# Kernel optimization log

Measured on AMD Instinct MI355X. Metric: run time of the kernel, lower is better.

Reference implementation:

```python
import jax, jax.numpy as jnp
import numpy as np


def setup_inputs() -> dict:
    key = jax.random.key(0)
    ks = jax.random.split(key, 3)
    B, d_in, d_latent = 8192, 768, 12288
    x = jax.random.normal(ks[0], (B, d_in), dtype=jnp.float32)
    # kaiming_normal fan_in relu: std = sqrt(2/d_in)
    W_enc = jax.random.normal(ks[1], (d_latent, d_in), dtype=jnp.float32) * np.sqrt(2.0 / d_in)
    b_enc = jnp.zeros((d_latent,), dtype=jnp.float32)
    # xavier_normal: std = sqrt(2/(d_in+d_latent))
    W_dec = jax.random.normal(ks[2], (d_in, d_latent), dtype=jnp.float32) * np.sqrt(2.0 / (d_in + d_latent))
    b_dec = jnp.zeros((d_in,), dtype=jnp.float32)
    b_pre = jnp.zeros((d_in,), dtype=jnp.float32)
    return {"x": x, "b_pre": b_pre, "W_enc": W_enc, "b_enc": b_enc,
            "W_dec": W_dec, "b_dec": b_dec, "k": 64}


def reference(x, b_pre, W_enc, b_enc, W_dec, b_dec, k):
    # encode: a = (x - b_pre) @ W_enc.T + b_enc   -> (B, d_latent)
    x0 = x - b_pre
    a = jnp.einsum('bi,li->bl', x0, W_enc) + b_enc
    # topk activation (mode='value', nonneg=True): relu then keep k largest
    a_relu = jax.nn.relu(a)
    topk_val, topk_idx = jax.lax.top_k(a_relu, k)  # (B, k)
    B = a.shape[0]
    rows = jnp.arange(B)[:, None]
    z = jnp.zeros_like(a).at[rows, topk_idx].set(topk_val)
    # decode: x_hat = z @ W_dec.T + b_dec
    x_hat = jnp.einsum('bl,il->bi', z, W_dec) + b_dec
    return (x_hat, z, a)
```

## Files before the change

kernel.cpp:

```cpp
#include <hip/hip_runtime.h>

#define DIN 768
#define DL  12288
#define CAP 320
#define CAP2 512
#define WCAP 256
#define TCAND 2.9f
#define MARGIN 0.03f
#define UB 0.015f
#define UMAX 64
#define KMAX 128

typedef __attribute__((ext_vector_type(8))) _Float16 half8;
typedef __attribute__((ext_vector_type(4))) _Float16 half4v;
typedef __attribute__((ext_vector_type(4))) float f32x4;

__device__ __forceinline__ void gl_lds16(const void* g, void* s) {
  __builtin_amdgcn_global_load_lds(
      (const __attribute__((address_space(1))) unsigned int*)g,
      (__attribute__((address_space(3))) unsigned int*)s, 16, 0, 0);
}
__device__ __forceinline__ void wait_lgkm0_fence() {
  asm volatile("s_waitcnt lgkmcnt(0)" ::: "memory");
  __builtin_amdgcn_sched_barrier(0);
}
__device__ __forceinline__ void wait_vm0() {
  asm volatile("s_waitcnt vmcnt(0)" ::: "memory");
}

#define NBX (8192 * DIN / 1024)
#define NBW (DL * DIN / 1024)
#define NBT ((DL / 32) * (DIN / 32))

template <int ZMETA>
__global__ __launch_bounds__(256) void k_prep(
    const float* __restrict__ x, const float* __restrict__ b_pre,
    const float* __restrict__ W_enc, const float* __restrict__ W_dec,
    _Float16* __restrict__ Ah, _Float16* __restrict__ Bh, _Float16* __restrict__ WT,
    int* __restrict__ meta)
{
  const int b = blockIdx.x, tid = threadIdx.x;
  if (b < NBX) {
    const int i4 = b * 256 + tid;
    const int col4 = (i4 % (DIN / 4)) * 4;
    const float4 xv = *(const float4*)&x[(size_t)i4 * 4];
    const float4 bp = *(const float4*)&b_pre[col4];
    half4v o;
    o.x = (_Float16)(xv.x - bp.x);
    o.y = (_Float16)(xv.y - bp.y);
    o.z = (_Float16)(xv.z - bp.z);
    o.w = (_Float16)(xv.w - bp.w);
    *(half4v*)&Ah[(size_t)i4 * 4] = o;
  } else if (b < NBX + NBW) {
    const int i4 = (b - NBX) * 256 + tid;
    const float4 wv = *(const float4*)&W_enc[(size_t)i4 * 4];
    half4v o;
    o.x = (_Float16)wv.x; o.y = (_Float16)wv.y;
    o.z = (_Float16)wv.z; o.w = (_Float16)wv.w;
    *(half4v*)&Bh[(size_t)i4 * 4] = o;
  } else if (b < NBX + NBW + NBT) {
    const int idx = b - NBX - NBW;
    const int c0 = (idx % (DL / 32)) * 32;
    const int r0 = (idx / (DL / 32)) * 32;
    const int xx = tid & 31, yy = tid >> 5;
    __shared__ float t[32][33];
#pragma unroll
    for (int dy = 0; dy < 32; dy += 8)
      t[yy + dy][xx] = W_dec[(size_t)(r0 + yy + dy) * DL + c0 + xx];
    __syncthreads();
#pragma unroll
    for (int dy = 0; dy < 32; dy += 8)
      WT[(size_t)(c0 + yy + dy) * DIN + r0 + xx] = (_Float16)t[xx][yy + dy];
  } else if (ZMETA) {
    const int4 z4 = {0, 0, 0, 0};
#pragma unroll
    for (int s = 0; s < 16; ++s) ((int4*)meta)[tid * 16 + s] = z4;
  }
}

#define BM 256
#define BN 256
#define BKE 64
#define NKT (DIN / BKE)

template <int EMIT>
__global__ __launch_bounds__(512) void k_encode_f16(
    const _Float16* __restrict__ Ah, const _Float16* __restrict__ Bh,
    const float* __restrict__ b_enc, float* __restrict__ aout,
    int* __restrict__ cnt, int2* __restrict__ cand)
{
  __shared__ _Float16 sA[2][BM][BKE];
  __shared__ _Float16 sB[2][BN][BKE];
  __shared__ int s_bcnt8[8];
  __shared__ int s_ovf;
  const int tid = threadIdx.x, wave = tid >> 6, lane = tid & 63;
  const int wm = wave >> 2, wn = wave & 3;
  const int fr = lane & 15, fc = lane >> 4;

  const int q = ((8192 / BM) * (DL / BN)) >> 3;
  const int wg = (blockIdx.x & 7) * q + (blockIdx.x >> 3);
  const int bm = (wg / (DL / BN)) * BM;
  const int bn = (wg % (DL / BN)) * BN;

  const int lrow = lane >> 3;
  const int lcol = ((lane & 7) ^ lrow) << 3;
  const _Float16* gA = Ah + (size_t)(bm + lrow) * DIN + lcol;
  const _Float16* gB = Bh + (size_t)(bn + lrow) * DIN + lcol;

  f32x4 acc[8][4];
#pragma unroll
  for (int i = 0; i < 8; ++i)
#pragma unroll
    for (int j = 0; j < 4; ++j) acc[i][j] = f32x4{0.f, 0.f, 0.f, 0.f};

#define STAGE_TILE(buf, tt)                                                      \
  {                                                                              \
    _Pragma("unroll")                                                            \
    for (int s4 = 0; s4 < 4; ++s4) {                                             \
      const int s8 = (wave + s4 * 8) * 8;                                        \
      gl_lds16(gA + (size_t)s8 * DIN + (tt) * BKE, &sA[buf][s8][0]);             \
      gl_lds16(gB + (size_t)s8 * DIN + (tt) * BKE, &sB[buf][s8][0]);             \
    }                                                                            \
  }

#define LOAD_AF(p, mh)                                                           \
  {                                                                              \
    const char* bA = (const char*)&sA[p][0][0];                                  \
    _Pragma("unroll")                                                            \
    for (int i = 0; i < 4; ++i)                                                  \
      _Pragma("unroll")                                                          \
      for (int ks = 0; ks < 2; ++ks) {                                           \
        const int row = wm * 128 + ((mh) * 4 + i) * 16 + fr;                     \
        const int ph = (ks * 4 + fc) ^ (fr & 7);                                 \
        af[i][ks] = *(const half8*)(bA + row * (BKE * 2) + ph * 16);             \
      }                                                                          \
  }
#define LOAD_BF(p, nh)                                                           \
  {                                                                              \
    const char* bB = (const char*)&sB[p][0][0];                                  \
    _Pragma("unroll")                                                            \
    for (int j = 0; j < 2; ++j)                                                  \
      _Pragma("unroll")                                                          \
      for (int ks = 0; ks < 2; ++ks) {                                           \
        const int row = wn * 64 + ((nh) * 2 + j) * 16 + fr;                      \
        const int ph = (ks * 4 + fc) ^ (fr & 7);                                 \
        bf[nh][j][ks] = *(const half8*)(bB + row * (BKE * 2) + ph * 16);         \
      }                                                                          \
  }

#define MFMAQ(mh, nh)                                                            \
  __builtin_amdgcn_s_setprio(1);                                                 \
  _Pragma("unroll")                                                              \
  for (int i = 0; i < 4; ++i)                                                    \
    _Pragma("unroll")                                                            \
    for (int j = 0; j < 2; ++j)                                                  \
      _Pragma("unroll")                                                          \
      for (int ks = 0; ks < 2; ++ks)                                             \
        acc[(mh) * 4 + i][(nh) * 2 + j] = __builtin_amdgcn_mfma_f32_16x16x32_f16( \
            af[i][ks], bf[nh][j][ks], acc[(mh) * 4 + i][(nh) * 2 + j], 0, 0, 0); \
  __builtin_amdgcn_s_setprio(0);

  half8 af[4][2], bf[2][2][2];

  STAGE_TILE(0, 0)
  wait_vm0();
  __builtin_amdgcn_s_barrier();

#pragma unroll 1
  for (int t = 0; t < NKT; ++t) {
    const int p = t & 1;
    LOAD_AF(p, 0)
    LOAD_BF(p, 0)
    if (t + 1 < NKT) STAGE_TILE(p ^ 1, t + 1)
    __builtin_amdgcn_s_barrier();
    wait_lgkm0_fence();
    MFMAQ(0, 0)
    __builtin_amdgcn_s_barrier();
    LOAD_BF(p, 1)
    __builtin_amdgcn_s_barrier();
    wait_lgkm0_fence();
    MFMAQ(0, 1)
    __builtin_amdgcn_s_barrier();
    LOAD_AF(p, 1)
    wait_vm0();
    __builtin_amdgcn_s_barrier();
    wait_lgkm0_fence();
    MFMAQ(1, 1)
    MFMAQ(1, 0)
    __builtin_amdgcn_s_barrier();
  }

  unsigned* pk   = (unsigned*)&sA[0][0][0];
  float*    pv   = (float*)&sA[1][0][0];
  int*      lcnt = (int*)&sB[0][0][0];
  if (EMIT) {
    if (tid < 8) s_bcnt8[tid] = 0;
    if (tid == 0) s_ovf = 0;
    if (tid < 256) lcnt[tid] = 0;
    __syncthreads();
  }

#pragma unroll
  for (int j = 0; j < 4; ++j) {
    const int col = bn + wn * 64 + j * 16 + fr;
    const float be = b_enc[col];
#pragma unroll
    for (int i = 0; i < 8; ++i) {
      const int row0 = bm + wm * 128 + i * 16 + fc * 4;
#pragma unroll
      for (int r = 0; r < 4; ++r) {
        const float v = acc[i][j][r] + be;
        aout[(size_t)(row0 + r) * DL + col] = v;
        if (EMIT && v > TCAND) {
          const int lr = wm * 128 + i * 16 + fc * 4 + r;
          const int lc = wn * 64 + j * 16 + fr;
          const int p2 = atomicAdd(&s_bcnt8[wave], 1);
          if (p2 < WCAP) {
            pk[wave * WCAP + p2] = ((unsigned)lr << 8) | (unsigned)lc;
            pv[wave * WCAP + p2] = v;
          }
          atomicAdd(&lcnt[lr], 1);
        }
      }
    }
  }

  if (EMIT) {
    __syncthreads();
    if (tid < 8 && s_bcnt8[tid] > WCAP) s_ovf = 1;
    __syncthreads();
    if (s_ovf) {
      if (tid < 256) atomicAdd(&cnt[bm + tid], CAP2);
    } else {
      if (tid < 256) {
        const int c = lcnt[tid];
        lcnt[tid] = c ? atomicAdd(&cnt[bm + tid], c) : 0;
      }
      __syncthreads();
#pragma unroll 1
      for (int w = 0; w < 8; ++w) {
        const int tw = s_bcnt8[w];
        for (int e = tid; e < tw; e += 512) {
          const unsigned pkv = pk[w * WCAP + e];
          const int lr = pkv >> 8, lc = pkv & 255u;
          const int p2 = atomicAdd(&lcnt[lr], 1);
          if (p2 < CAP2) {
            int2 o; o.x = __float_as_int(pv[w * WCAP + e]); o.y = bn + lc;
            cand[(size_t)(bm + lr) * CAP2 + p2] = o;
          }
        }
      }
    }
  }
#undef STAGE_TILE
#undef LOAD_AF
#undef LOAD_BF
#undef MFMAQ
}

__global__ __launch_bounds__(512) void k_fast(
    const int* __restrict__ cnt, const int2* __restrict__ cand,
    const float* __restrict__ x, const float* __restrict__ b_pre,
    const float* __restrict__ W, const float* __restrict__ b_enc,
    const int* __restrict__ kp, const _Float16* __restrict__ WT,
    const float* __restrict__ b_dec, float* __restrict__ z,
    float* __restrict__ xhat, int* __restrict__ flag)
{
  const int row = blockIdx.x, tid = threadIdx.x;
  const int wave = tid >> 6, lane = tid & 63;
  const int kk = min(max(kp[0], 1), KMAX);
  float* zr = z + (size_t)row * DL;

  __shared__ float cv[CAP2];
  __shared__ int ci[CAP2];
  __shared__ double x0[DIN];
  __shared__ float s_ak;
  __shared__ int s_nw, s_ucnt;
  __shared__ int uidx[UMAX];
  __shared__ double uex[UMAX];
  __shared__ int widx[KMAX];
  __shared__ float wval[KMAX];

  const float4 zz = {0.f, 0.f, 0.f, 0.f};
#pragma unroll
  for (int j = 0; j < 6; ++j) ((float4*)zr)[tid + 512 * j] = zz;

  const int Craw = cnt[row];
  const int C = min(Craw, CAP2);
  for (int i = tid; i < C; i += 512) {
    const int2 p = cand[(size_t)row * CAP2 + i];
    cv[i] = __int_as_float(p.x);
    ci[i] = p.y;
  }
  for (int i = tid; i < DIN; i += 512)
    x0[i] = (double)x[(size_t)row * DIN + i] - (double)b_pre[i];
  if (tid == 0) { s_ak = -1e30f; s_nw = 0; s_ucnt = 0; }
  __syncthreads();

  bool defic = (Craw >= CAP2) || (C < kk);
  if (!defic) {
    if (tid < C) {
      const float mv = cv[tid];
      const int mi = ci[tid];
      int r = 0;
      for (int j = 0; j < C; ++j) {
        const float fj = cv[j];
        if (fj > mv || (fj == mv && ci[j] < mi)) ++r;
      }
      if (r == kk - 1) s_ak = mv;
    }
    __syncthreads();
    if (s_ak - UB <= TCAND) defic = true;
  } else {
    __syncthreads();
  }
  if (defic) {
    if (tid == 0) flag[row] = 1;
    return;
  }
  const float ak = s_ak;

  if (tid < C) {
    const float mv = cv[tid];
    if (mv > ak + UB) {
      const int p = atomicAdd(&s_nw, 1);
      widx[p] = ci[tid]; wval[p] = mv;
    } else if (mv >= ak - UB) {
      const int p = atomicAdd(&s_ucnt, 1);
      if (p < UMAX) uidx[p] = ci[tid];
    }
  }
  __syncthreads();
  const int nci = s_nw;
  const int ucnt = min(s_ucnt, UMAX);

  for (int c = wave; c < ucnt; c += 8) {
    const int idx = uidx[c];
    const float* wrow = W + (size_t)idx * DIN;
    double s = 0.0;
#pragma unroll
    for (int it = 0; it < DIN / 64; ++it)
      s = fma(x0[lane + it * 64], (double)wrow[lane + it * 64], s);
#pragma unroll
    for (int mm = 32; mm; mm >>= 1) s += __shfl_xor(s, mm);
    if (lane == 0) {
      const double e = s + (double)b_enc[idx];
      uex[c] = e > 0.0 ? e : 0.0;
    }
  }
  __syncthreads();

  const int utake = min(kk - nci, ucnt);
  if (tid < ucnt) {
    const double mv = uex[tid];
    const int mi = uidx[tid];
    int r = 0;
    for (int j = 0; j < ucnt; ++j) {
      const double fj = uex[j];
      if (fj > mv || (fj == mv && uidx[j] < mi)) ++r;
    }
    if (r < utake) {
      const int p = atomicAdd(&s_nw, 1);
      widx[p] = mi; wval[p] = (float)mv;
    }
  }
  __syncthreads();
  const int nW = s_nw;

  if (tid < nW) zr[widx[tid]] = wval[tid];

  if (tid < 192) {
    float4 acc = ((const float4*)b_dec)[tid];
    for (int j = 0; j < nW; ++j) {
      const float vv = wval[j];
      const half4v w4 = *(const half4v*)(WT + (size_t)widx[j] * DIN + tid * 4);
      acc.x = fmaf(vv, (float)w4.x, acc.x);
      acc.y = fmaf(vv, (float)w4.y, acc.y);
      acc.z = fmaf(vv, (float)w4.z, acc.z);
      acc.w = fmaf(vv, (float)w4.w, acc.w);
    }
    ((float4*)(xhat + (size_t)row * DIN))[tid] = acc;
  }
}

template <int FORCE_ALL, int ZERO_Z>
__global__ __launch_bounds__(512) void k_full(
    const float* __restrict__ a, const float* __restrict__ x,
    const float* __restrict__ b_pre, const float* __restrict__ W,
    const float* __restrict__ b_enc, const int* __restrict__ kp,
    const _Float16* __restrict__ WT, const float* __restrict__ b_dec,
    float* __restrict__ z, float* __restrict__ xhat, const int* __restrict__ flag)
{
  const int row = blockIdx.x, tid = threadIdx.x;
  if (!FORCE_ALL && flag[row] == 0) return;
  const int wave = tid >> 6, lane = tid & 63;
  const int kk = min(max(kp[0], 1), KMAX);
  const float* ar = a + (size_t)row * DL;
  float* zr = z + (size_t)row * DL;

  __shared__ unsigned hist[4][512];
  __shared__ float s_wmax[8];
  __shared__ unsigned s_wsuf[8];
  __shared__ float s_Tm;
  __shared__ int s_cnt;
  __shared__ int cidx[CAP];
  __shared__ float caf[CAP];
  __shared__ double x0[DIN];
  __shared__ float s_ak;
  __shared__ int s_ucnt, s_nw;
  __shared__ int uidx[UMAX];
  __shared__ double uex[UMAX];
  __shared__ int widx[KMAX];
  __shared__ float wval[KMAX];

  float4 v[6];
#pragma unroll
  for (int j = 0; j < 6; ++j) {
    float4 t4 = ((const float4*)ar)[tid + 512 * j];
    t4.x = fmaxf(t4.x, 0.f); t4.y = fmaxf(t4.y, 0.f);
    t4.z = fmaxf(t4.z, 0.f); t4.w = fmaxf(t4.w, 0.f);
    v[j] = t4;
    if (ZERO_Z) {
      const float4 zz = {0.f, 0.f, 0.f, 0.f};
      ((float4*)zr)[tid + 512 * j] = zz;
    }
  }
  for (int i = tid; i < DIN; i += 512)
    x0[i] = (double)x[(size_t)row * DIN + i] - (double)b_pre[i];
  float m = 0.f;
#pragma unroll
  for (int j = 0; j < 6; ++j)
    m = fmaxf(m, fmaxf(fmaxf(v[j].x, v[j].y), fmaxf(v[j].z, v[j].w)));
#pragma unroll
  for (int off = 32; off; off >>= 1) m = fmaxf(m, __shfl_xor(m, off));
  if (lane == 0) s_wmax[wave] = m;
  if (tid == 0) { s_cnt = 0; s_Tm = -1.f; s_ak = -1e30f; s_ucnt = 0; s_nw = 0; }
  __syncthreads();
  float rmax = s_wmax[0];
#pragma unroll
  for (int w2 = 1; w2 < 8; ++w2) rmax = fmaxf(rmax, s_wmax[w2]);

  float Tm;
  if (rmax <= 0.f) {
    Tm = 1e30f;
  } else {
    const float scale = 512.f / rmax;
    unsigned need = (unsigned)kk;
    bool found = false;
    for (int phase = 0; phase < 2 && !found; ++phase) {
      for (int i = tid; i < 4 * 512; i += 512) (&hist[0][0])[i] = 0u;
      __syncthreads();
      unsigned* h = hist[wave & 3];
      const float sc = (phase == 0) ? scale : scale * 8.f;
#pragma unroll
      for (int j = 0; j < 6; ++j) {
        const float vv[4] = {v[j].x, v[j].y, v[j].z, v[j].w};
#pragma unroll
        for (int e = 0; e < 4; ++e) {
          const float val = vv[e];
          if (val > 0.f) {
            const float fb = val * scale;
            if (phase == 0) {
              if (fb >= 64.f) atomicAdd(&h[min(511, (int)fb)], 1u);
            } else {
              if (fb < 64.f) atomicAdd(&h[min(511, (int)(val * sc))], 1u);
            }
          }
        }
      }
      __syncthreads();
      const unsigned st = hist[0][tid] + hist[1][tid] + hist[2][tid] + hist[3][tid];
      unsigned s = st;
#pragma unroll
      for (int off = 1; off < 64; off <<= 1) {
        const unsigned o = __shfl_down(s, off);
        if (lane + off < 64) s += o;
      }
      if (lane == 0) s_wsuf[wave] = s;
      __syncthreads();
      unsigned above_w = 0, total = 0;
#pragma unroll
      for (int w2 = 0; w2 < 8; ++w2) {
        total += s_wsuf[w2];
        if (w2 > wave) above_w += s_wsuf[w2];
      }
      const unsigned inc = s + above_w;
      const unsigned excl = inc - st;
      if (total >= need) {
        if (inc >= need && excl < need)
          s_Tm = (float)tid / sc - MARGIN;
        found = true;
      } else {
        need -= total;
      }
      __syncthreads();
    }
    Tm = s_Tm;
  }

#pragma unroll
  for (int j = 0; j < 6; ++j) {
    const float vv[4] = {v[j].x, v[j].y, v[j].z, v[j].w};
#pragma unroll
    for (int e = 0; e < 4; ++e) {
      if (vv[e] > 0.f && vv[e] >= Tm) {
        const int p = atomicAdd(&s_cnt, 1);
        if (p < CAP) { cidx[p] = (tid + 512 * j) * 4 + e; caf[p] = vv[e]; }
      }
    }
  }
  __syncthreads();
  const int C = min(s_cnt, CAP);

  if (C > kk) {
    if (tid < C) {
      const float mv = caf[tid];
      const int mi = cidx[tid];
      int r = 0;
      for (int j = 0; j < C; ++j) {
        const float fj = caf[j];
        if (fj > mv || (fj == mv && cidx[j] < mi)) ++r;
      }
      if (r == kk - 1) s_ak = mv;
    }
    __syncthreads();
  }
  const float ak = s_ak;

  if (tid < C) {
    const float mv = caf[tid];
    if (C <= kk || mv > ak + UB) {
      const int p = atomicAdd(&s_nw, 1);
      widx[p] = cidx[tid]; wval[p] = mv;
    } else if (mv >= ak - UB) {
      const int p = atomicAdd(&s_ucnt, 1);
      if (p < UMAX) uidx[p] = cidx[tid];
    }
  }
  __syncthreads();
  const int nci = s_nw;
  const int ucnt = min(s_ucnt, UMAX);

  for (int c = wave; c < ucnt; c += 8) {
    const int idx = uidx[c];
    const float* wrow = W + (size_t)idx * DIN;
    double s = 0.0;
#pragma unroll
    for (int it = 0; it < DIN / 64; ++it)
      s = fma(x0[lane + it * 64], (double)wrow[lane + it * 64], s);
#pragma unroll
    for (int mm = 32; mm; mm >>= 1) s += __shfl_xor(s, mm);
    if (lane == 0) {
      const double e = s + (double)b_enc[idx];
      uex[c] = e > 0.0 ? e : 0.0;
    }
  }
  __syncthreads();

  const int utake = min(kk - nci, ucnt);
  if (tid < ucnt) {
    const double mv = uex[tid];
    const int mi = uidx[tid];
    int r = 0;
    for (int j = 0; j < ucnt; ++j) {
      const double fj = uex[j];
      if (fj > mv || (fj == mv && uidx[j] < mi)) ++r;
    }
    if (r < utake) {
      const int p = atomicAdd(&s_nw, 1);
      widx[p] = mi; wval[p] = (float)mv;
    }
  }
  __syncthreads();
  const int nW = s_nw;

  if (tid < nW) zr[widx[tid]] = wval[tid];

  if (tid < 192) {
    float4 acc = ((const float4*)b_dec)[tid];
    for (int j = 0; j < nW; ++j) {
      const float vv = wval[j];
      const half4v w4 = *(const half4v*)(WT + (size_t)widx[j] * DIN + tid * 4);
      acc.x = fmaf(vv, (float)w4.x, acc.x);
      acc.y = fmaf(vv, (float)w4.y, acc.y);
      acc.z = fmaf(vv, (float)w4.z, acc.z);
      acc.w = fmaf(vv, (float)w4.w, acc.w);
    }
    ((float4*)(xhat + (size_t)row * DIN))[tid] = acc;
  }
}

extern "C" void kernel_launch(void* const* d_in, const int* in_sizes, int n_in,
                              void* d_out, int out_size, void* d_ws, size_t ws_size,
                              hipStream_t stream)
{
  const float* x     = (const float*)d_in[0];
  const float* b_pre = (const float*)d_in[1];
  const float* W_enc = (const float*)d_in[2];
  const float* b_enc = (const float*)d_in[3];
  const float* W_dec = (const float*)d_in[4];
  const float* b_dec = (const float*)d_in[5];
  const int*   kp    = (const int*)d_in[6];
  const int M = in_sizes[0] / DIN;

  float* xhat = (float*)d_out;
  float* z    = xhat + (size_t)M * DIN;
  float* a    = z + (size_t)M * DL;

  const bool bigws = ws_size >= ((size_t)192 << 20);

  if (bigws) {
    int*      cnt  = (int*)d_ws;
    int*      flag = (int*)d_ws + M;
    int2*     cand = (int2*)((char*)d_ws + ((size_t)1 << 20));
    _Float16* WT16 = (_Float16*)((char*)d_ws + ((size_t)40 << 20));
    _Float16* Ah   = (_Float16*)((char*)d_ws + ((size_t)64 << 20));
    _Float16* Bh   = (_Float16*)((char*)d_ws + ((size_t)96 << 20));

    k_prep<1><<<NBX + NBW + NBT + 1, 256, 0, stream>>>(x, b_pre, W_enc, W_dec,
                                                       Ah, Bh, WT16, cnt);
    k_encode_f16<1><<<(M / BM) * (DL / BN), 512, 0, stream>>>(Ah, Bh, b_enc, a,
                                                              cnt, cand);
    k_fast<<<M, 512, 0, stream>>>(cnt, cand, x, b_pre, W_enc, b_enc, kp, WT16, b_dec,
                                  z, xhat, flag);
    k_full<0, 0><<<M, 512, 0, stream>>>(a, x, b_pre, W_enc, b_enc, kp, WT16, b_dec,
                                        z, xhat, flag);
  } else {
    _Float16* WT16 = (_Float16*)z;
    _Float16* Ah   = (_Float16*)(z + (size_t)12 * 1024 * 1024);
    _Float16* Bh   = (_Float16*)(z + (size_t)20 * 1024 * 1024);

    k_prep<0><<<NBX + NBW + NBT, 256, 0, stream>>>(x, b_pre, W_enc, W_dec,
                                                   Ah, Bh, WT16, nullptr);
    k_encode_f16<0><<<(M / BM) * (DL / BN), 512, 0, stream>>>(Ah, Bh, b_enc, a,
                                                              nullptr, nullptr);
    k_full<1, 1><<<M, 512, 0, stream>>>(a, x, b_pre, W_enc, b_enc, kp, WT16, b_dec,
                                        z, xhat, nullptr);
  }
}
```

Measured before the change: 630.7 us.

## Merge fast and fallback top-k kernels; simplify encode GEMM barriers

```diff
diff --git a/kernel.cpp b/kernel.cpp
--- a/kernel.cpp
+++ b/kernel.cpp
@@ -19,13 +19,6 @@
   __builtin_amdgcn_global_load_lds(
       (const __attribute__((address_space(1))) unsigned int*)g,
       (__attribute__((address_space(3))) unsigned int*)s, 16, 0, 0);
-}
-__device__ __forceinline__ void wait_lgkm0_fence() {
-  asm volatile("s_waitcnt lgkmcnt(0)" ::: "memory");
-  __builtin_amdgcn_sched_barrier(0);
-}
-__device__ __forceinline__ void wait_vm0() {
-  asm volatile("s_waitcnt vmcnt(0)" ::: "memory");
 }
 
 #define NBX (8192 * DIN / 1024)
@@ -74,7 +67,7 @@
   } else if (ZMETA) {
     const int4 z4 = {0, 0, 0, 0};
 #pragma unroll
-    for (int s = 0; s < 16; ++s) ((int4*)meta)[tid * 16 + s] = z4;
+    for (int s = 0; s < 8; ++s) ((int4*)meta)[tid * 8 + s] = z4;
   }
 }
 
@@ -163,8 +156,7 @@
   half8 af[4][2], bf[2][2][2];
 
   STAGE_TILE(0, 0)
-  wait_vm0();
-  __builtin_amdgcn_s_barrier();
+  __syncthreads();
 
 #pragma unroll 1
   for (int t = 0; t < NKT; ++t) {
@@ -172,22 +164,13 @@
     LOAD_AF(p, 0)
     LOAD_BF(p, 0)
     if (t + 1 < NKT) STAGE_TILE(p ^ 1, t + 1)
-    __builtin_amdgcn_s_barrier();
-    wait_lgkm0_fence();
     MFMAQ(0, 0)
-    __builtin_amdgcn_s_barrier();
     LOAD_BF(p, 1)
-    __builtin_amdgcn_s_barrier();
-    wait_lgkm0_fence();
     MFMAQ(0, 1)
-    __builtin_amdgcn_s_barrier();
     LOAD_AF(p, 1)
-    wait_vm0();
-    __builtin_amdgcn_s_barrier();
-    wait_lgkm0_fence();
     MFMAQ(1, 1)
     MFMAQ(1, 0)
-    __builtin_amdgcn_s_barrier();
+    __syncthreads();
   }
 
   unsigned* pk   = (unsigned*)&sA[0][0][0];
@@ -258,13 +241,13 @@
 #undef MFMAQ
 }
 
-__global__ __launch_bounds__(512) void k_fast(
+__global__ __launch_bounds__(512) void k_back(
     const int* __restrict__ cnt, const int2* __restrict__ cand,
-    const float* __restrict__ x, const float* __restrict__ b_pre,
-    const float* __restrict__ W, const float* __restrict__ b_enc,
-    const int* __restrict__ kp, const _Float16* __restrict__ WT,
-    const float* __restrict__ b_dec, float* __restrict__ z,
-    float* __restrict__ xhat, int* __restrict__ flag)
+    const float* __restrict__ a, const float* __restrict__ x,
+    const float* __restrict__ b_pre, const float* __restrict__ W,
+    const float* __restrict__ b_enc, const int* __restrict__ kp,
+    const _Float16* __restrict__ WT, const float* __restrict__ b_dec,
+    float* __restrict__ z, float* __restrict__ xhat)
 {
   const int row = blockIdx.x, tid = threadIdx.x;
   const int wave = tid >> 6, lane = tid & 63;
@@ -275,18 +258,22 @@
   __shared__ int ci[CAP2];
   __shared__ double x0[DIN];
   __shared__ float s_ak;
-  __shared__ int s_nw, s_ucnt;
+  __shared__ int s_nw, s_ucnt, s_cnt2;
   __shared__ int uidx[UMAX];
   __shared__ double uex[UMAX];
   __shared__ int widx[KMAX];
   __shared__ float wval[KMAX];
+  __shared__ unsigned hist[4][512];
+  __shared__ float s_wmax[8];
+  __shared__ unsigned s_wsuf[8];
+  __shared__ float s_Tm;
 
   const float4 zz = {0.f, 0.f, 0.f, 0.f};
 #pragma unroll
   for (int j = 0; j < 6; ++j) ((float4*)zr)[tid + 512 * j] = zz;
 
   const int Craw = cnt[row];
-  const int C = min(Craw, CAP2);
+  int C = min(Craw, CAP2);
   for (int i = tid; i < C; i += 512) {
     const int2 p = cand[(size_t)row * CAP2 + i];
     cv[i] = __int_as_float(p.x);
@@ -314,15 +301,122 @@
   } else {
     __syncthreads();
   }
+  float ak = s_ak;
+
   if (defic) {
-    if (tid == 0) flag[row] = 1;
-    return;
-  }
-  const float ak = s_ak;
+    const float* ar = a + (size_t)row * DL;
+    float4 v[6];
+#pragma unroll
+    for (int j = 0; j < 6; ++j) {
+      float4 t4 = ((const float4*)ar)[tid + 512 * j];
+      t4.x = fmaxf(t4.x, 0.f); t4.y = fmaxf(t4.y, 0.f);
+      t4.z = fmaxf(t4.z, 0.f); t4.w = fmaxf(t4.w, 0.f);
+      v[j] = t4;
+    }
+    float m = 0.f;
+#pragma unroll
+    for (int j = 0; j < 6; ++j)
+      m = fmaxf(m, fmaxf(fmaxf(v[j].x, v[j].y), fmaxf(v[j].z, v[j].w)));
+#pragma unroll
+    for (int off = 32; off; off >>= 1) m = fmaxf(m, __shfl_xor(m, off));
+    if (lane == 0) s_wmax[wave] = m;
+    if (tid == 0) { s_cnt2 = 0; s_Tm = -1.f; s_ak = -1e30f; s_nw = 0; s_ucnt = 0; }
+    __syncthreads();
+    float rmax = s_wmax[0];
+#pragma unroll
+    for (int w2 = 1; w2 < 8; ++w2) rmax = fmaxf(rmax, s_wmax[w2]);
+
+    float Tm;
+    if (rmax <= 0.f) {
+      Tm = 1e30f;
+    } else {
+      const float scale = 512.f / rmax;
+      unsigned need = (unsigned)kk;
+      bool found = false;
+      for (int phase = 0; phase < 2 && !found; ++phase) {
+        for (int i = tid; i < 4 * 512; i += 512) (&hist[0][0])[i] = 0u;
+        __syncthreads();
+        unsigned* h = hist[wave & 3];
+        const float sc = (phase == 0) ? scale : scale * 8.f;
+#pragma unroll
+        for (int j = 0; j < 6; ++j) {
+          const float vv[4] = {v[j].x, v[j].y, v[j].z, v[j].w};
+#pragma unroll
+          for (int e = 0; e < 4; ++e) {
+            const float val = vv[e];
+            if (val > 0.f) {
+              const float fb = val * scale;
+              if (phase == 0) {
+                if (fb >= 64.f) atomicAdd(&h[min(511, (int)fb)], 1u);
+              } else {
+                if (fb < 64.f) atomicAdd(&h[min(511, (int)(val * sc))], 1u);
+              }
+            }
+          }
+        }
+        __syncthreads();
+        const unsigned st = hist[0][tid] + hist[1][tid] + hist[2][tid] + hist[3][tid];
+        unsigned s = st;
+#pragma unroll
+        for (int off = 1; off < 64; off <<= 1) {
+          const unsigned o = __shfl_down(s, off);
+          if (lane + off < 64) s += o;
+        }
+        if (lane == 0) s_wsuf[wave] = s;
+        __syncthreads();
+        unsigned above_w = 0, total = 0;
+#pragma unroll
+        for (int w2 = 0; w2 < 8; ++w2) {
+          total += s_wsuf[w2];
+          if (w2 > wave) above_w += s_wsuf[w2];
+        }
+        const unsigned inc = s + above_w;
+        const unsigned excl = inc - st;
+        if (total >= need) {
+          if (inc >= need && excl < need)
+            s_Tm = (float)tid / sc - MARGIN;
+          found = true;
+        } else {
+          need -= total;
+        }
+        __syncthreads();
+      }
+      Tm = s_Tm;
+    }
+
+#pragma unroll
+    for (int j = 0; j < 6; ++j) {
+      const float vv[4] = {v[j].x, v[j].y, v[j].z, v[j].w};
+#pragma unroll
+      for (int e = 0; e < 4; ++e) {
+        if (vv[e] > 0.f && vv[e] >= Tm) {
+          const int p = atomicAdd(&s_cnt2, 1);
+          if (p < CAP) { ci[p] = (tid + 512 * j) * 4 + e; cv[p] = vv[e]; }
+        }
+      }
+    }
+    __syncthreads();
+    C = min(s_cnt2, CAP);
+
+    if (C > kk) {
+      if (tid < C) {
+        const float mv = cv[tid];
+        const int mi = ci[tid];
+        int r = 0;
+        for (int j = 0; j < C; ++j) {
+          const float fj = cv[j];
+          if (fj > mv || (fj == mv && ci[j] < mi)) ++r;
+        }
+        if (r == kk - 1) s_ak = mv;
+      }
+      __syncthreads();
+    }
+    ak = s_ak;
+  }
 
   if (tid < C) {
     const float mv = cv[tid];
-    if (mv > ak + UB) {
+    if (C <= kk || mv > ak + UB) {
       const int p = atomicAdd(&s_nw, 1);
       widx[p] = ci[tid]; wval[p] = mv;
     } else if (mv >= ak - UB) {
@@ -383,16 +477,14 @@
   }
 }
 
-template <int FORCE_ALL, int ZERO_Z>
 __global__ __launch_bounds__(512) void k_full(
     const float* __restrict__ a, const float* __restrict__ x,
     const float* __restrict__ b_pre, const float* __restrict__ W,
     const float* __restrict__ b_enc, const int* __restrict__ kp,
     const _Float16* __restrict__ WT, const float* __restrict__ b_dec,
-    float* __restrict__ z, float* __restrict__ xhat, const int* __restrict__ flag)
+    float* __restrict__ z, float* __restrict__ xhat)
 {
   const int row = blockIdx.x, tid = threadIdx.x;
-  if (!FORCE_ALL && flag[row] == 0) return;
   const int wave = tid >> 6, lane = tid & 63;
   const int kk = min(max(kp[0], 1), KMAX);
   const float* ar = a + (size_t)row * DL;
@@ -420,10 +512,8 @@
     t4.x = fmaxf(t4.x, 0.f); t4.y = fmaxf(t4.y, 0.f);
     t4.z = fmaxf(t4.z, 0.f); t4.w = fmaxf(t4.w, 0.f);
     v[j] = t4;
-    if (ZERO_Z) {
-      const float4 zz = {0.f, 0.f, 0.f, 0.f};
-      ((float4*)zr)[tid + 512 * j] = zz;
-    }
+    const float4 zz = {0.f, 0.f, 0.f, 0.f};
+    ((float4*)zr)[tid + 512 * j] = zz;
   }
   for (int i = tid; i < DIN; i += 512)
     x0[i] = (double)x[(size_t)row * DIN + i] - (double)b_pre[i];
@@ -611,7 +701,6 @@
 
   if (bigws) {
     int*      cnt  = (int*)d_ws;
-    int*      flag = (int*)d_ws + M;
     int2*     cand = (int2*)((char*)d_ws + ((size_t)1 << 20));
     _Float16* WT16 = (_Float16*)((char*)d_ws + ((size_t)40 << 20));
     _Float16* Ah   = (_Float16*)((char*)d_ws + ((size_t)64 << 20));
@@ -621,10 +710,8 @@
                                                        Ah, Bh, WT16, cnt);
     k_encode_f16<1><<<(M / BM) * (DL / BN), 512, 0, stream>>>(Ah, Bh, b_enc, a,
                                                               cnt, cand);
-    k_fast<<<M, 512, 0, stream>>>(cnt, cand, x, b_pre, W_enc, b_enc, kp, WT16, b_dec,
-                                  z, xhat, flag);
-    k_full<0, 0><<<M, 512, 0, stream>>>(a, x, b_pre, W_enc, b_enc, kp, WT16, b_dec,
-                                        z, xhat, flag);
+    k_back<<<M, 512, 0, stream>>>(cnt, cand, a, x, b_pre, W_enc, b_enc, kp,
+                                  WT16, b_dec, z, xhat);
   } else {
     _Float16* WT16 = (_Float16*)z;
     _Float16* Ah   = (_Float16*)(z + (size_t)12 * 1024 * 1024);
@@ -634,7 +721,7 @@
                                                    Ah, Bh, WT16, nullptr);
     k_encode_f16<0><<<(M / BM) * (DL / BN), 512, 0, stream>>>(Ah, Bh, b_enc, a,
                                                               nullptr, nullptr);
-    k_full<1, 1><<<M, 512, 0, stream>>>(a, x, b_pre, W_enc, b_enc, kp, WT16, b_dec,
-                                        z, xhat, nullptr);
+    k_full<<<M, 512, 0, stream>>>(a, x, b_pre, W_enc, b_enc, kp, WT16, b_dec,
+                                  z, xhat);
   }
 }
```

Measured after the change: 655.4 us. 1.04x slower.
